# Kernel optimization log

Measured on AMD Instinct MI355X. Metric: run time of the kernel, lower is better.

## Reference

```python
import jax, jax.numpy as jnp
import numpy as np

V = 64                 # |Sigma|
IN_DIM = V + 2         # Sigma + '(' + ')'
OUT_DIM = V + 1        # Sigma + <del>/<end>
H = 512
B = 256
SX = 34                # max proto length 32 + 2 boundaries
SY = 34
BIG_NEG = -1000000000.0


def _one_hot_seq(key, S, batch):
    # '(' at pos 0, L random symbols, ')' at pos L+1, zero padding after
    kl, ks = jax.random.split(key)
    lengths = jax.random.randint(kl, (batch,), 4, S - 1)        # L in [4, S-2]
    syms = jax.random.randint(ks, (S, batch), 0, V)
    pos = jnp.arange(S)[:, None]
    tok = jnp.where(pos == 0, V, jnp.where(pos == lengths[None, :] + 1, V + 1, syms))
    oh = jax.nn.one_hot(tok, IN_DIM, dtype=jnp.float32)
    valid = (pos <= lengths[None, :] + 1).astype(jnp.float32)
    return oh * valid[:, :, None]


def setup_inputs() -> dict:
    key = jax.random.key(0)
    ks = jax.random.split(key, 14)

    def p(k, shape, scale):
        return jax.random.uniform(k, shape, jnp.float32, -scale, scale)

    s = 1.0 / float(np.sqrt(H))
    s2 = 1.0 / float(np.sqrt(2 * H))
    return {
        "sources": _one_hot_seq(ks[0], SX, B),
        "targets": _one_hot_seq(ks[1], SY, B),
        # bidirectional prior LSTM (input IN_DIM -> hidden H, fwd + rev)
        "Wih_f": p(ks[2], (4 * H, IN_DIM), s), "Whh_f": p(ks[3], (4 * H, H), s), "b_f": p(ks[4], (4 * H,), s),
        "Wih_r": p(ks[5], (4 * H, IN_DIM), s), "Whh_r": p(ks[6], (4 * H, H), s), "b_r": p(ks[7], (4 * H,), s),
        # modern LSTM (input IN_DIM -> hidden 2H)
        "Wih_m": p(ks[8], (8 * H, IN_DIM), s2), "Whh_m": p(ks[9], (8 * H, 2 * H), s2), "b_m": p(ks[10], (8 * H,), s2),
        # heads: Linear(2H -> OUT_DIM) + LogSoftmax
        "W_sub": p(ks[11], (OUT_DIM, 2 * H), s2), "b_sub": jnp.zeros((OUT_DIM,), jnp.float32),
        "W_ins": p(ks[12], (OUT_DIM, 2 * H), s2), "b_ins": jnp.zeros((OUT_DIM,), jnp.float32),
    }


def _lstm(x, Wih, Whh, b, hid):
    # torch gate order: i, f, g, o
    bsz = x.shape[1]
    def step(carry, xt):
        h, c = carry
        g = xt @ Wih.T + h @ Whh.T + b
        i, f, gg, o = jnp.split(g, 4, axis=-1)
        c = jax.nn.sigmoid(f) * c + jax.nn.sigmoid(i) * jnp.tanh(gg)
        h = jax.nn.sigmoid(o) * jnp.tanh(c)
        return (h, c), h
    init = (jnp.zeros((bsz, hid), x.dtype), jnp.zeros((bsz, hid), x.dtype))
    _, hs = jax.lax.scan(step, init, x)
    return hs  # [S, B, hid]


def _forward(sources, targets, Wih_f, Whh_f, b_f, Wih_r, Whh_r, b_r,
             Wih_m, Whh_m, b_m, W_sub, b_sub, W_ins, b_ins):
    x_fwd = _lstm(sources, Wih_f, Whh_f, b_f, H)
    x_bwd = _lstm(sources[::-1], Wih_r, Whh_r, b_r, H)[::-1]
    x_emb = jnp.concatenate([x_fwd, x_bwd], axis=-1)   # [SX, B, 2H]
    y_emb = _lstm(targets, Wih_m, Whh_m, b_m, 2 * H)    # [SY, B, 2H]

    # head(x_emb[i] + y_emb[j]) decomposes since Linear is affine
    def pair_logprobs(W, bb):
        lx = jnp.einsum('ibh,oh->ibo', x_emb, W)              # [SX, B, O]
        ly = jnp.einsum('jbh,oh->jbo', y_emb, W) + bb         # [SY, B, O]
        return jax.nn.log_softmax(lx[:, None] + ly[None, :], axis=-1)  # [SX, SY, B, O]

    sub_log = pair_logprobs(W_sub, b_sub)
    ins_log = pair_logprobs(W_ins, b_ins)

    # cell (i, j, b) is computed iff x[i] and y[j] are real (non-padding) one-hots, j <= max_cognat_length
    x_any = sources.sum(-1) > 0                                # [SX, B]
    y_any = targets.sum(-1) > 0                                # [SY, B]
    j_ok = jnp.arange(SY) < SY - 1
    valid = x_any[:, None, :] & (y_any & j_ok[:, None])[None, :, :]   # [SX, SY, B]

    end = jnp.where(valid, ins_log[..., V], BIG_NEG)           # insProbs[V_SIZE]
    dlt = jnp.where(valid, sub_log[..., V], BIG_NEG)           # subProbs[V_SIZE]

    y_next = jnp.pad(targets[1:], ((0, 1), (0, 0), (0, 0)))    # y[j+1], [SY, B, IN_DIM]
    ins_ok = valid & (y_next[..., IN_DIM - 1] == 0)[None]      # not bool(y[j+1, V_SIZE+1])
    ins_val = jnp.einsum('ijbv,jbv->ijb', ins_log[..., :V], y_next[..., :V])
    sub_val = jnp.einsum('ijbv,jbv->ijb', sub_log[..., :V], y_next[..., :V])

    # stacked cached probs: [ins, sub, end, del], each [SX, SY, B]
    return jnp.stack([
        jnp.where(ins_ok, ins_val, BIG_NEG),
        jnp.where(ins_ok, sub_val, BIG_NEG),
        end,
        dlt,
    ])


def reference(sources, targets, Wih_f, Whh_f, b_f, Wih_r, Whh_r, b_r,
              Wih_m, Whh_m, b_m, W_sub, b_sub, W_ins, b_ins):
    return _forward(sources, targets, Wih_f, Whh_f, b_f, Wih_r, Whh_r, b_r,
                    Wih_m, Whh_m, b_m, W_sub, b_sub, W_ins, b_ins)
```

## Files before the change

kernel.cpp:

```cpp
#include <hip/hip_runtime.h>

typedef __attribute__((ext_vector_type(4))) float f32x4;
typedef unsigned char u8;
typedef unsigned long long u64t;

#define BIG_NEG -1000000000.0f

static constexpr int B_  = 256;
static constexpr int SX_ = 34;
static constexpr int SY_ = 34;
static constexpr int IND = 66;
static constexpr int OP_ = 80;

__device__ __forceinline__ f32x4 mfma_fp8(long a, long b, f32x4 c) {
  return __builtin_amdgcn_mfma_f32_16x16x32_fp8_fp8(a, b, c, 0, 0, 0);
}
__device__ __forceinline__ float sigm(float x)  { return 1.0f / (1.0f + __expf(-x)); }
__device__ __forceinline__ float tanhx(float x) { return 2.0f * sigm(2.0f * x) - 1.0f; }
template <bool HI>
__device__ __forceinline__ unsigned pk2(float a, float b, unsigned old) {
  return __builtin_amdgcn_cvt_pk_fp8_f32(a, b, (int)old, HI);
}
__device__ __forceinline__ long pack8(const float* p) {
  float4 f0 = *(const float4*)p;
  float4 f1 = *(const float4*)(p + 4);
  unsigned w0 = pk2<false>(f0.x, f0.y, 0); w0 = pk2<true>(f0.z, f0.w, w0);
  unsigned w1 = pk2<false>(f1.x, f1.y, 0); w1 = pk2<true>(f1.z, f1.w, w1);
  return (long)(((u64t)w1 << 32) | (u64t)w0);
}

__global__ __launch_bounds__(256) void prep_all(
    const float* __restrict__ src, const float* __restrict__ tgt,
    int* __restrict__ tok_x, int* __restrict__ tok_y,
    const float* __restrict__ Wsub, const float* __restrict__ Wins,
    u8* __restrict__ Wcat,
    const float* __restrict__ Wihf, const float* __restrict__ bf,
    const float* __restrict__ Wihr, const float* __restrict__ br,
    const float* __restrict__ Wihm, const float* __restrict__ bm,
    float* __restrict__ Ef, float* __restrict__ Er, float* __restrict__ Em,
    const float* __restrict__ Whm, u8* __restrict__ w8m) {
  __shared__ float tile[64 * 67];
  const int blk = blockIdx.x;
  const int tid = threadIdx.x;

  if (blk < 68) {
    int idx = blk * 256 + tid;
    const int half = SX_ * B_;
    const float* base = (idx < half) ? src : tgt;
    int* outp         = (idx < half) ? tok_x : tok_y;
    int k = (idx < half) ? idx : idx - half;
    const float* p = base + (size_t)k * IND;
    int tok = -1;
    for (int v = 0; v < IND; ++v) if (p[v] > 0.5f) tok = v;
    outp[k] = tok;
  } else if (blk < 228) {
    int widx = (blk - 68) * 256 + tid;
    int row = widx >> 8;
    int wc  = widx & 255;
    int srow = row < 80 ? row : row - 80;
    const float* W = row < 80 ? Wsub : Wins;
    float f0 = 0.f, f1 = 0.f, f2 = 0.f, f3 = 0.f;
    if (srow < 65) {
      const float* p = W + (size_t)srow * 1024 + wc * 4;
      f0 = p[0]; f1 = p[1]; f2 = p[2]; f3 = p[3];
    }
    unsigned w = pk2<false>(f0, f1, 0);
    w = pk2<true>(f2, f3, w);
    ((unsigned*)Wcat)[widx] = w;
  } else if (blk < 356) {
    int tb = blk - 228;
    const float* W; const float* bias; float* E; int H4; int n0;
    if (tb < 32)      { W = Wihf; bias = bf; E = Ef; H4 = 2048; n0 = tb * 64; }
    else if (tb < 64) { W = Wihr; bias = br; E = Er; H4 = 2048; n0 = (tb - 32) * 64; }
    else              { W = Wihm; bias = bm; E = Em; H4 = 4096; n0 = (tb - 64) * 64; }
    const float* s2 = W + (size_t)n0 * IND;
    for (int i = tid; i < 64 * IND; i += 256) {
      int n = i / IND, v = i - n * IND;
      tile[n * 67 + v] = s2[i];
    }
    __syncthreads();
    int lane = tid & 63, w2 = tid >> 6;
    float bl = bias[n0 + lane];
    for (int v = w2; v < 67; v += 4) {
      float val = (v < 66 ? tile[lane * 67 + v] : 0.f) + bl;
      E[(size_t)v * H4 + n0 + lane] = val;
    }
  } else {
    const int M4 = 4096 * 1024 / 4;
    int i = (blk - 356) * 256 + tid;
    int stride = 3072 * 256;
    for (; i < M4; i += stride) {
      float4 f = ((const float4*)Whm)[i];
      unsigned w3 = pk2<false>(f.x, f.y, 0);
      w3 = pk2<true>(f.z, f.w, w3);
      ((unsigned*)w8m)[i] = w3;
    }
  }
}

__device__ __forceinline__ void run_lstm_mod(
    const u8* __restrict__ w8, const float* __restrict__ E,
    u8* __restrict__ hall, int b0, int h0,
    unsigned* __restrict__ dom_flags, int myid,
    u8* __restrict__ alds, u8* __restrict__ hT, const u8* __restrict__ tok_small) {
  constexpr int HH = 1024;
  constexpr int NS = 32;
  const int tid = threadIdx.x;
  const int lane = tid & 63, w = tid >> 6;
  const int lo = lane & 15, q = lane >> 4;
  constexpr int AST2 = HH + 8;
  constexpr int NK = HH / 32;
  const int hh = lo & 7;
  const bool hi = (lo >= 8);
  const int hu_e = h0 + w * 8 + hh;

  long breg0[NK], breg1[NK];
  {
    const u8* brow0 = w8 + (size_t)((lo >> 3) * HH + hu_e) * HH + q * 8;
    const u8* brow1 = w8 + (size_t)((2 + (lo >> 3)) * HH + hu_e) * HH + q * 8;
#pragma unroll
    for (int kk = 0; kk < NK; ++kk) {
      breg0[kk] = *(const long*)(brow0 + kk * 32);
      breg1[kk] = *(const long*)(brow1 + kk * 32);
    }
  }
  float creg[4] = {0.f, 0.f, 0.f, 0.f};

  for (int t = 0; t < 34; ++t) {
    f32x4 acc[2][2];
#pragma unroll
    for (int mt = 0; mt < 2; ++mt) {
      acc[mt][0] = (f32x4){0.f, 0.f, 0.f, 0.f};
      acc[mt][1] = (f32x4){0.f, 0.f, 0.f, 0.f};
    }

    if (t > 0) {
      const u8* hsrc = hall + (size_t)t * (256 * HH);
      u64t tmp[16];
#pragma unroll
      for (int ii = 0; ii < 16; ++ii) {
        int idx = tid + ii * 256;
        tmp[ii] = __hip_atomic_load(
            (const u64t*)(hsrc + (size_t)(b0 + (idx >> 7)) * HH + (idx & 127) * 8),
            __ATOMIC_RELAXED, __HIP_MEMORY_SCOPE_AGENT);
      }
#pragma unroll
      for (int ii = 0; ii < 16; ++ii) {
        int idx = tid + ii * 256;
        *(u64t*)&alds[(idx >> 7) * AST2 + (idx & 127) * 8] = tmp[ii];
      }
      __syncthreads();

      const u8* a0p = alds + lo * AST2 + q * 8;
      const u8* a1p = alds + (16 + lo) * AST2 + q * 8;
#pragma unroll
      for (int kk = 0; kk < NK; ++kk) {
        long a0 = *(const long*)(a0p + kk * 32);
        long a1 = *(const long*)(a1p + kk * 32);
        acc[0][0] = mfma_fp8(a0, breg0[kk], acc[0][0]);
        acc[0][1] = mfma_fp8(a0, breg1[kk], acc[0][1]);
        acc[1][0] = mfma_fp8(a1, breg0[kk], acc[1][0]);
        acc[1][1] = mfma_fp8(a1, breg1[kk], acc[1][1]);
      }
    }

    const u8* tkp = tok_small + t * 32;
#pragma unroll
    for (int mt = 0; mt < 2; ++mt) {
      f32x4 t0 = acc[mt][0], t1 = acc[mt][1];
      f32x4 p0, p1;
#pragma unroll
      for (int c2 = 0; c2 < 4; ++c2) {
        p0[c2] = __shfl_xor(t0[c2], 8, 64);
        p1[c2] = __shfl_xor(t1[c2], 8, 64);
      }
#pragma unroll
      for (int rr = 0; rr < 2; ++rr) {
        int r = (hi ? 2 : 0) + rr;
        float iv = hi ? p0[r] : t0[r];
        float fv = hi ? t0[r] : p0[r];
        float gv = hi ? p1[r] : t1[r];
        float ov = hi ? t1[r] : p1[r];
        int m = mt * 16 + q * 4 + r;
        int v = tkp[m];
        const float* e = E + (size_t)v * (4 * HH) + hu_e;
        iv += e[0]; fv += e[HH]; gv += e[2 * HH]; ov += e[3 * HH];
        float cold = creg[mt * 2 + rr];
        float cn = sigm(fv) * cold + sigm(iv) * tanhx(gv);
        float hn = sigm(ov) * tanhx(cn);
        creg[mt * 2 + rr] = cn;
        hT[m * 32 + w * 8 + hh] = (u8)(pk2<false>(hn, hn, 0) & 0xffu);
      }
    }
    __syncthreads();

    {
      int m = tid >> 3, cc = tid & 7;
      unsigned val = *(const unsigned*)&hT[m * 32 + cc * 4];
      u8* hdst = hall + (size_t)(t + 1) * (256 * HH);
      __hip_atomic_store((unsigned*)(hdst + (size_t)(b0 + m) * HH + h0 + cc * 4),
                         val, __ATOMIC_RELAXED, __HIP_MEMORY_SCOPE_AGENT);
    }

    if (t < 33) {
      __asm__ volatile("s_waitcnt vmcnt(0)" ::: "memory");
      __syncthreads();
      unsigned tgt = (unsigned)(t + 1);
      if (tid == 0)
        __hip_atomic_store(&dom_flags[myid * 32], tgt,
                           __ATOMIC_RELAXED, __HIP_MEMORY_SCOPE_AGENT);
      if (tid < NS) {
        int spin = 0;
        for (;;) {
          unsigned v = __hip_atomic_load(&dom_flags[tid * 32],
                                         __ATOMIC_RELAXED, __HIP_MEMORY_SCOPE_AGENT);
          if (__ballot(v < tgt) == 0) break;
          __builtin_amdgcn_s_sleep(1);
          if (++spin > (1 << 17)) break;
        }
      }
      __syncthreads();
    }
  }
}

__device__ __forceinline__ void run_lstm_fr(
    const float* __restrict__ Whh, const float* __restrict__ E,
    bool revr, u8* __restrict__ hall, int b0, int h0,
    unsigned* __restrict__ dom_flags, int myid,
    u8* __restrict__ alds, u8* __restrict__ hT, const u8* __restrict__ tok_small) {
  constexpr int HH = 512;
  constexpr int NS = 16;
  const int tid = threadIdx.x;
  const int lane = tid & 63, w = tid >> 6;
  const int lo = lane & 15, q = lane >> 4;
  constexpr int AST2 = HH + 8;
  const int hh = lo & 7;
  const bool hi = (lo >= 8);
  const int hu_e = h0 + w * 8 + hh;

  long breg0[16], breg1[16];
  {
    const float* bf0 = Whh + ((size_t)((lo >> 3) * HH + hu_e)) * HH + q * 8;
    const float* bf1 = Whh + ((size_t)((2 + (lo >> 3)) * HH + hu_e)) * HH + q * 8;
#pragma unroll
    for (int kk = 0; kk < 16; ++kk) {
      breg0[kk] = pack8(bf0 + kk * 32);
      breg1[kk] = pack8(bf1 + kk * 32);
    }
  }
  float creg[4] = {0.f, 0.f, 0.f, 0.f};

  for (int t = 0; t < 34; ++t) {
    f32x4 acc[2][2];
#pragma unroll
    for (int mt = 0; mt < 2; ++mt) {
      acc[mt][0] = (f32x4){0.f, 0.f, 0.f, 0.f};
      acc[mt][1] = (f32x4){0.f, 0.f, 0.f, 0.f};
    }

    if (t > 0) {
      const u8* hsrc = hall + (size_t)t * (256 * HH);
      u64t tmp[8];
#pragma unroll
      for (int ii = 0; ii < 8; ++ii) {
        int idx = tid + ii * 256;
        tmp[ii] = __hip_atomic_load(
            (const u64t*)(hsrc + (size_t)(b0 + (idx >> 6)) * HH + (idx & 63) * 8),
            __ATOMIC_RELAXED, __HIP_MEMORY_SCOPE_AGENT);
      }
#pragma unroll
      for (int ii = 0; ii < 8; ++ii) {
        int idx = tid + ii * 256;
        *(u64t*)&alds[(idx >> 6) * AST2 + (idx & 63) * 8] = tmp[ii];
      }
      __syncthreads();

      const u8* a0p = alds + lo * AST2 + q * 8;
      const u8* a1p = alds + (16 + lo) * AST2 + q * 8;
#pragma unroll
      for (int kk = 0; kk < 16; ++kk) {
        long a0 = *(const long*)(a0p + kk * 32);
        long a1 = *(const long*)(a1p + kk * 32);
        acc[0][0] = mfma_fp8(a0, breg0[kk], acc[0][0]);
        acc[0][1] = mfma_fp8(a0, breg1[kk], acc[0][1]);
        acc[1][0] = mfma_fp8(a1, breg0[kk], acc[1][0]);
        acc[1][1] = mfma_fp8(a1, breg1[kk], acc[1][1]);
      }
    }

    int tpos = revr ? 33 - t : t;
    const u8* tkp = tok_small + tpos * 32;
#pragma unroll
    for (int mt = 0; mt < 2; ++mt) {
      f32x4 t0 = acc[mt][0], t1 = acc[mt][1];
      f32x4 p0, p1;
#pragma unroll
      for (int c2 = 0; c2 < 4; ++c2) {
        p0[c2] = __shfl_xor(t0[c2], 8, 64);
        p1[c2] = __shfl_xor(t1[c2], 8, 64);
      }
#pragma unroll
      for (int rr = 0; rr < 2; ++rr) {
        int r = (hi ? 2 : 0) + rr;
        float iv = hi ? p0[r] : t0[r];
        float fv = hi ? t0[r] : p0[r];
        float gv = hi ? p1[r] : t1[r];
        float ov = hi ? t1[r] : p1[r];
        int m = mt * 16 + q * 4 + r;
        int v = tkp[m];
        const float* e = E + (size_t)v * (4 * HH) + hu_e;
        iv += e[0]; fv += e[HH]; gv += e[2 * HH]; ov += e[3 * HH];
        float cold = creg[mt * 2 + rr];
        float cn = sigm(fv) * cold + sigm(iv) * tanhx(gv);
        float hn = sigm(ov) * tanhx(cn);
        creg[mt * 2 + rr] = cn;
        hT[m * 32 + w * 8 + hh] = (u8)(pk2<false>(hn, hn, 0) & 0xffu);
      }
    }
    __syncthreads();

    {
      int m = tid >> 3, cc = tid & 7;
      unsigned val = *(const unsigned*)&hT[m * 32 + cc * 4];
      u8* hdst = hall + (size_t)(t + 1) * (256 * HH);
      __hip_atomic_store((unsigned*)(hdst + (size_t)(b0 + m) * HH + h0 + cc * 4),
                         val, __ATOMIC_RELAXED, __HIP_MEMORY_SCOPE_AGENT);
    }

    if (t < 33) {
      __asm__ volatile("s_waitcnt vmcnt(0)" ::: "memory");
      __syncthreads();
      unsigned tgt = (unsigned)(t + 1);
      if (tid == 0)
        __hip_atomic_store(&dom_flags[myid * 32], tgt,
                           __ATOMIC_RELAXED, __HIP_MEMORY_SCOPE_AGENT);
      if (tid < NS) {
        int spin = 0;
        for (;;) {
          unsigned v = __hip_atomic_load(&dom_flags[tid * 32],
                                         __ATOMIC_RELAXED, __HIP_MEMORY_SCOPE_AGENT);
          if (__ballot(v < tgt) == 0) break;
          __builtin_amdgcn_s_sleep(1);
          if (++spin > (1 << 17)) break;
        }
      }
      __syncthreads();
    }
  }
}

__global__ __launch_bounds__(256, 2) void lstm_persist(
    const int* __restrict__ tok_x, const int* __restrict__ tok_y,
    const float* __restrict__ E_f, const float* __restrict__ Whh_f,
    const float* __restrict__ E_r, const float* __restrict__ Whh_r,
    const float* __restrict__ E_m, const u8* __restrict__ w8_m,
    u8* __restrict__ fwd_all, u8* __restrict__ rev_all, u8* __restrict__ y_all,
    unsigned* __restrict__ flags) {
  __shared__ u8 alds[32 * 1032];
  __shared__ u8 hT[32 * 32];
  __shared__ u8 tok_small[34 * 32];

  const int b = blockIdx.x;
  int role, c, s;
  if (b < 256)      { role = 2; c = b >> 5; s = b & 31; }
  else if (b < 384) { int l = b - 256; role = 0; c = l >> 4; s = l & 15; }
  else              { int l = b - 384; role = 1; c = l >> 4; s = l & 15; }

  u8* hall        = role == 0 ? fwd_all : role == 1 ? rev_all : y_all;
  const int* tokg = (role == 2) ? tok_y : tok_x;
  const int b0 = c * 32;
  const int h0 = s * 32;
  const int dom0 = (role == 2) ? c * 32 : (role == 0) ? 256 + c * 16 : 384 + c * 16;

  for (int i = threadIdx.x; i < 34 * 32; i += 256) {
    int t2 = i >> 5, m = i & 31;
    int tk = tokg[t2 * 256 + b0 + m];
    tok_small[i] = (u8)(tk < 0 ? 66 : tk);
  }
  __syncthreads();

  unsigned* dom_flags = flags + dom0 * 32;
  if (role == 2)
    run_lstm_mod(w8_m, E_m, hall, b0, h0, dom_flags, s, alds, hT, tok_small);
  else if (role == 0)
    run_lstm_fr(Whh_f, E_f, false, hall, b0, h0, dom_flags, s, alds, hT, tok_small);
  else
    run_lstm_fr(Whh_r, E_r, true, hall, b0, h0, dom_flags, s, alds, hT, tok_small);
}

__global__ __launch_bounds__(256, 1) void head_kernel(
    const u8* __restrict__ fwd_all, const u8* __restrict__ rev_all,
    const u8* __restrict__ y_all, const u8* __restrict__ Wcat,
    const float* __restrict__ b_sub, const float* __restrict__ b_ins,
    float* __restrict__ lx_sub, float* __restrict__ lx_ins,
    float* __restrict__ ly_sub, float* __restrict__ ly_ins) {
  __shared__ u8 wq[160 * 264];
  const int lane = threadIdx.x & 63, wave = threadIdx.x >> 6;
  const int lo = lane & 15, q = lane >> 4;
  int blk = blockIdx.x;
  bool yside = (blk >= 136);
  int mb = yside ? blk - 136 : blk;
  int ij = mb >> 2;
  int bbase = (mb & 3) * 64;

  f32x4 acc[10];
#pragma unroll
  for (int nn = 0; nn < 10; ++nn) acc[nn] = (f32x4){0.f,0.f,0.f,0.f};

  for (int qk = 0; qk < 4; ++qk) {
    long aA[8];
    {
      int row = bbase + wave * 16 + lo;
      const u8* ab;
      if (yside)
        ab = y_all + ((size_t)(ij + 1) * 256 + row) * 1024 + qk * 256 + q * 8;
      else if (qk < 2)
        ab = fwd_all + ((size_t)(ij + 1) * 256 + row) * 512 + qk * 256 + q * 8;
      else
        ab = rev_all + ((size_t)(34 - ij) * 256 + row) * 512 + (qk - 2) * 256 + q * 8;
#pragma unroll
      for (int ki = 0; ki < 8; ++ki) aA[ki] = *(const long*)(ab + ki * 32);
    }

    for (int c8 = threadIdx.x; c8 < 160 * 32; c8 += 256) {
      int row = c8 >> 5, col = (c8 & 31) << 3;
      *(long*)&wq[row * 264 + col] =
          *(const long*)&Wcat[(size_t)row * 1024 + qk * 256 + col];
    }
    __syncthreads();

#pragma unroll
    for (int ki = 0; ki < 8; ++ki) {
#pragma unroll
      for (int nn = 0; nn < 10; ++nn) {
        long bf = *(const long*)&wq[(nn * 16 + lo) * 264 + ki * 32 + q * 8];
        acc[nn] = mfma_fp8(aA[ki], bf, acc[nn]);
      }
    }
    __syncthreads();
  }

#pragma unroll
  for (int nn = 0; nn < 10; ++nn) {
    bool is_sub = (nn < 5);
    int n = (is_sub ? nn : nn - 5) * 16 + lo;
    float bias = 0.0f;
    if (yside && n < 65) bias = is_sub ? b_sub[n] : b_ins[n];
    float* dst = yside ? (is_sub ? ly_sub : ly_ins) : (is_sub ? lx_sub : lx_ins);
#pragma unroll
    for (int r = 0; r < 4; ++r) {
      int b = bbase + wave * 16 + q * 4 + r;
      dst[((size_t)ij * 256 + b) * OP_ + n] = acc[nn][r] + bias;
    }
  }
}

__device__ __forceinline__ void lse_one(const float4* __restrict__ X,
                                        const float* __restrict__ py, int sym,
                                        float& logZ, float& v64, float& vs) {
  float v[68];
  const float4* py4 = (const float4*)py;
#pragma unroll
  for (int q = 0; q < 17; ++q) {
    float4 yb = py4[q];
    v[4 * q + 0] = X[q].x + yb.x;
    v[4 * q + 1] = X[q].y + yb.y;
    v[4 * q + 2] = X[q].z + yb.z;
    v[4 * q + 3] = X[q].w + yb.w;
  }
  float m = v[0];
#pragma unroll
  for (int o = 1; o < 65; ++o) m = fmaxf(m, v[o]);
  float s = 0.0f, vsl = 0.0f;
#pragma unroll
  for (int o = 0; o < 65; ++o) {
    s += __expf(v[o] - m);
    if (o < 64) vsl = (o == sym) ? v[o] : vsl;
  }
  logZ = m + __logf(s);
  v64 = v[64];
  vs = vsl;
}

__global__ __launch_bounds__(256, 1) void pair_kernel(
    const int* __restrict__ tok_x, const int* __restrict__ tok_y,
    const float* __restrict__ lx_sub, const float* __restrict__ lx_ins,
    const float* __restrict__ ly_sub, const float* __restrict__ ly_ins,
    float* __restrict__ out) {
  const int hsel = blockIdx.x >= 136;
  const int rem = hsel ? blockIdx.x - 136 : blockIdx.x;
  const int i = rem >> 2;
  const int bc = rem & 3;
  const int jq = threadIdx.x >> 6;
  const int bl = threadIdx.x & 63;
  const int b = bc * 64 + bl;
  const size_t CH = (size_t)SX_ * SY_ * B_;
  const float* lx = hsel ? lx_ins : lx_sub;
  const float* ly = hsel ? ly_ins : ly_sub;
  float* outA = out + (hsel ? 0 : CH);
  float* outB = out + (hsel ? 2 * CH : 3 * CH);

  float4 X[17];
  {
    const float4* ps = (const float4*)(lx + ((size_t)i * 256 + b) * OP_);
#pragma unroll
    for (int q = 0; q < 17; ++q) X[q] = ps[q];
  }
  int tx = tok_x[i * 256 + b];

  for (int j = jq; j < 34; j += 4) {
    size_t obase = ((size_t)i * SY_ + j) * 256 + b;
    bool dead = (j == SY_ - 1) || (tx < 0);
    if (!dead) {
      int ty = tok_y[j * 256 + b];
      if (ty < 0) dead = true;
    }
    if (dead) {
      outA[obase] = BIG_NEG;
      outB[obase] = BIG_NEG;
      continue;
    }
    int tn = tok_y[(j + 1) * 256 + b];
    bool ins_ok = (tn != 65);
    int sym = (tn >= 0 && tn < 64) ? tn : -1;

    float logZ, v64, vs;
    lse_one(X, ly + ((size_t)j * 256 + b) * OP_, sym, logZ, v64, vs);
    float valB = v64 - logZ;
    float valA = (sym >= 0) ? (vs - logZ) : 0.0f;
    outA[obase] = ins_ok ? valA : BIG_NEG;
    outB[obase] = valB;
  }
}

extern "C" void kernel_launch(void* const* d_in, const int* in_sizes, int n_in,
                              void* d_out, int out_size, void* d_ws, size_t ws_size,
                              hipStream_t stream) {
  const float* sources = (const float*)d_in[0];
  const float* targets = (const float*)d_in[1];
  const float* Wih_f = (const float*)d_in[2];
  const float* Whh_f = (const float*)d_in[3];
  const float* b_f   = (const float*)d_in[4];
  const float* Wih_r = (const float*)d_in[5];
  const float* Whh_r = (const float*)d_in[6];
  const float* b_r   = (const float*)d_in[7];
  const float* Wih_m = (const float*)d_in[8];
  const float* Whh_m = (const float*)d_in[9];
  const float* b_m   = (const float*)d_in[10];
  const float* W_sub = (const float*)d_in[11];
  const float* b_sub = (const float*)d_in[12];
  const float* W_ins = (const float*)d_in[13];
  const float* b_ins = (const float*)d_in[14];
  float* out = (float*)d_out;

  char* w = (char*)d_ws;
  constexpr size_t FLAG_SZ = 512 * 32 * 4;
  constexpr size_t TOK_SZ  = (size_t)SX_ * B_ * 4;
  constexpr size_t WCAT_SZ = (size_t)160 * 1024;
  constexpr size_t W8M_SZ  = (size_t)4096 * 1024;
  constexpr size_t EF_SZ   = (size_t)67 * 2048 * 4;
  constexpr size_t EM_SZ   = (size_t)67 * 4096 * 4;
  constexpr size_t LX_SZ   = (size_t)SX_ * B_ * OP_ * 4;
  constexpr size_t HF_SZ   = (size_t)35 * B_ * 512;
  constexpr size_t HM_SZ   = (size_t)35 * B_ * 1024;

  size_t off = 0;
  unsigned* flags = (unsigned*)(w + off); off += FLAG_SZ;
  int*  tok_x   = (int*)(w + off);  off += TOK_SZ;
  int*  tok_y   = (int*)(w + off);  off += TOK_SZ;
  off = (off + 255) & ~(size_t)255;
  u8*   Wcat    = (u8*)(w + off);   off += WCAT_SZ;
  u8*   w8_m    = (u8*)(w + off);   off += W8M_SZ;
  float* E_f    = (float*)(w + off); off += EF_SZ;
  float* E_r    = (float*)(w + off); off += EF_SZ;
  float* E_m    = (float*)(w + off); off += EM_SZ;
  float* lx_sub = (float*)(w + off); off += LX_SZ;
  float* lx_ins = (float*)(w + off); off += LX_SZ;
  float* ly_sub = (float*)(w + off); off += LX_SZ;
  float* ly_ins = (float*)(w + off); off += LX_SZ;
  u8* fwd_all   = (u8*)(w + off);   off += HF_SZ;
  u8* rev_all   = (u8*)(w + off);   off += HF_SZ;
  u8* y_all     = (u8*)(w + off);   off += HM_SZ;
  (void)ws_size; (void)in_sizes; (void)n_in; (void)out_size;

  (void)hipMemsetAsync(flags, 0, FLAG_SZ, stream);

  prep_all<<<3428, 256, 0, stream>>>(
      sources, targets, tok_x, tok_y,
      W_sub, W_ins, Wcat,
      Wih_f, b_f, Wih_r, b_r, Wih_m, b_m, E_f, E_r, E_m,
      Whh_m, w8_m);

  lstm_persist<<<512, 256, 0, stream>>>(
      tok_x, tok_y,
      E_f, Whh_f,
      E_r, Whh_r,
      E_m, w8_m,
      fwd_all, rev_all, y_all, flags);

  head_kernel<<<272, 256, 0, stream>>>(fwd_all, rev_all, y_all, Wcat,
                                       b_sub, b_ins, lx_sub, lx_ins, ly_sub, ly_ins);

  pair_kernel<<<272, 256, 0, stream>>>(tok_x, tok_y, lx_sub, lx_ins,
                                       ly_sub, ly_ins, out);
}
```

Before: 341.0 us.

## Fold input projection into fp8 MFMA via one-hot augmented K, store y-logits as bf16

Instead of gathering fp32 input-projection rows (plus bias) from a precomputed table per timestep, the one-hot token and a constant-1 column are written into an extra 96-byte K segment of the LDS A tile. The matching fp8 Wih and bias columns are appended as three extra MFMA K-steps held in registers. This removes the scattered global gathers in the gate epilogue. The cost is fp8 quantization of Wih and bias, extra register pressure, and a slightly larger LDS tile. Separately, the y-side head logits are stored as bf16 to halve the traffic read by pair_kernel, at some precision loss.

```diff
diff --git a/kernel.cpp b/kernel.cpp
--- a/kernel.cpp
+++ b/kernel.cpp
@@ -2,6 +2,7 @@
 
 typedef __attribute__((ext_vector_type(4))) float f32x4;
 typedef unsigned char u8;
+typedef unsigned short u16;
 typedef unsigned long long u64t;
 
 #define BIG_NEG -1000000000.0f
@@ -11,6 +12,7 @@
 static constexpr int SY_ = 34;
 static constexpr int IND = 66;
 static constexpr int OP_ = 80;
+static constexpr int KE_ = 96;
 
 __device__ __forceinline__ f32x4 mfma_fp8(long a, long b, f32x4 c) {
   return __builtin_amdgcn_mfma_f32_16x16x32_fp8_fp8(a, b, c, 0, 0, 0);
@@ -27,6 +29,13 @@
   unsigned w0 = pk2<false>(f0.x, f0.y, 0); w0 = pk2<true>(f0.z, f0.w, w0);
   unsigned w1 = pk2<false>(f1.x, f1.y, 0); w1 = pk2<true>(f1.z, f1.w, w1);
   return (long)(((u64t)w1 << 32) | (u64t)w0);
+}
+__device__ __forceinline__ u16 f2bf(float f) {
+  unsigned b = __float_as_uint(f) + 0x8000u;
+  return (u16)(b >> 16);
+}
+__device__ __forceinline__ float bf2f(unsigned us) {
+  return __uint_as_float(us << 16);
 }
 
 __global__ __launch_bounds__(256) void prep_all(
@@ -37,9 +46,8 @@
     const float* __restrict__ Wihf, const float* __restrict__ bf,
     const float* __restrict__ Wihr, const float* __restrict__ br,
     const float* __restrict__ Wihm, const float* __restrict__ bm,
-    float* __restrict__ Ef, float* __restrict__ Er, float* __restrict__ Em,
+    u8* __restrict__ w8e,
     const float* __restrict__ Whm, u8* __restrict__ w8m) {
-  __shared__ float tile[64 * 67];
   const int blk = blockIdx.x;
   const int tid = threadIdx.x;
 
@@ -67,28 +75,37 @@
     unsigned w = pk2<false>(f0, f1, 0);
     w = pk2<true>(f2, f3, w);
     ((unsigned*)Wcat)[widx] = w;
-  } else if (blk < 356) {
-    int tb = blk - 228;
-    const float* W; const float* bias; float* E; int H4; int n0;
-    if (tb < 32)      { W = Wihf; bias = bf; E = Ef; H4 = 2048; n0 = tb * 64; }
-    else if (tb < 64) { W = Wihr; bias = br; E = Er; H4 = 2048; n0 = (tb - 32) * 64; }
-    else              { W = Wihm; bias = bm; E = Em; H4 = 4096; n0 = (tb - 64) * 64; }
-    const float* s2 = W + (size_t)n0 * IND;
-    for (int i = tid; i < 64 * IND; i += 256) {
-      int n = i / IND, v = i - n * IND;
-      tile[n * 67 + v] = s2[i];
-    }
-    __syncthreads();
-    int lane = tid & 63, w2 = tid >> 6;
-    float bl = bias[n0 + lane];
-    for (int v = w2; v < 67; v += 4) {
-      float val = (v < 66 ? tile[lane * 67 + v] : 0.f) + bl;
-      E[(size_t)v * H4 + n0 + lane] = val;
+  } else if (blk < 268) {
+    int row = (blk - 228) * 256 + tid;
+    if (row < 8192) {
+      const float* W; const float* bias; int r;
+      if (row < 2048)      { W = Wihf; bias = bf; r = row; }
+      else if (row < 4096) { W = Wihr; bias = br; r = row - 2048; }
+      else                 { W = Wihm; bias = bm; r = row - 4096; }
+      const float* wr = W + (size_t)r * IND;
+      float bv = bias[r];
+      unsigned* dst = (unsigned*)(w8e + (size_t)row * KE_);
+#pragma unroll
+      for (int w4 = 0; w4 < 24; ++w4) {
+        float v0 = 0.f, v1 = 0.f, v2 = 0.f, v3 = 0.f;
+        int c = w4 * 4;
+        if (c + 3 < 66) {
+          v0 = wr[c]; v1 = wr[c + 1]; v2 = wr[c + 2]; v3 = wr[c + 3];
+        } else if (c < 68) {
+          v0 = (c < 66) ? wr[c] : (c == 66 ? bv : 0.f);
+          v1 = (c + 1 < 66) ? wr[c + 1] : (c + 1 == 66 ? bv : 0.f);
+          v2 = (c + 2 < 66) ? wr[c + 2] : (c + 2 == 66 ? bv : 0.f);
+          v3 = (c + 3 < 66) ? wr[c + 3] : (c + 3 == 66 ? bv : 0.f);
+        }
+        unsigned w2 = pk2<false>(v0, v1, 0);
+        w2 = pk2<true>(v2, v3, w2);
+        dst[w4] = w2;
+      }
     }
   } else {
     const int M4 = 4096 * 1024 / 4;
-    int i = (blk - 356) * 256 + tid;
-    int stride = 3072 * 256;
+    int i = (blk - 268) * 256 + tid;
+    int stride = 3160 * 256;
     for (; i < M4; i += stride) {
       float4 f = ((const float4*)Whm)[i];
       unsigned w3 = pk2<false>(f.x, f.y, 0);
@@ -99,22 +116,22 @@
 }
 
 __device__ __forceinline__ void run_lstm_mod(
-    const u8* __restrict__ w8, const float* __restrict__ E,
+    const u8* __restrict__ w8, const u8* __restrict__ w8e,
     u8* __restrict__ hall, int b0, int h0,
     unsigned* __restrict__ dom_flags, int myid,
     u8* __restrict__ alds, u8* __restrict__ hT, const u8* __restrict__ tok_small) {
   constexpr int HH = 1024;
   constexpr int NS = 32;
+  constexpr int NK = 32;
   const int tid = threadIdx.x;
   const int lane = tid & 63, w = tid >> 6;
   const int lo = lane & 15, q = lane >> 4;
-  constexpr int AST2 = HH + 8;
-  constexpr int NK = HH / 32;
+  constexpr int AST2 = HH + KE_ + 8;
   const int hh = lo & 7;
   const bool hi = (lo >= 8);
   const int hu_e = h0 + w * 8 + hh;
 
-  long breg0[NK], breg1[NK];
+  long breg0[NK + 3], breg1[NK + 3];
   {
     const u8* brow0 = w8 + (size_t)((lo >> 3) * HH + hu_e) * HH + q * 8;
     const u8* brow1 = w8 + (size_t)((2 + (lo >> 3)) * HH + hu_e) * HH + q * 8;
@@ -123,17 +140,25 @@
       breg0[kk] = *(const long*)(brow0 + kk * 32);
       breg1[kk] = *(const long*)(brow1 + kk * 32);
     }
+    const u8* e0 = w8e + (size_t)((lo >> 3) * HH + hu_e) * KE_ + q * 8;
+    const u8* e1 = w8e + (size_t)((2 + (lo >> 3)) * HH + hu_e) * KE_ + q * 8;
+#pragma unroll
+    for (int e = 0; e < 3; ++e) {
+      breg0[NK + e] = *(const long*)(e0 + e * 32);
+      breg1[NK + e] = *(const long*)(e1 + e * 32);
+    }
   }
   float creg[4] = {0.f, 0.f, 0.f, 0.f};
 
   for (int t = 0; t < 34; ++t) {
-    f32x4 acc[2][2];
-#pragma unroll
-    for (int mt = 0; mt < 2; ++mt) {
-      acc[mt][0] = (f32x4){0.f, 0.f, 0.f, 0.f};
-      acc[mt][1] = (f32x4){0.f, 0.f, 0.f, 0.f};
-    }
-
+    if (tid < 32) {
+      u8* rowp = alds + tid * AST2 + HH;
+#pragma unroll
+      for (int w8i = 0; w8i < 12; ++w8i) *(u64t*)(rowp + 8 * w8i) = 0;
+      int v = tok_small[t * 32 + tid];
+      if (v < 66) rowp[v] = 0x38;
+      rowp[66] = 0x38;
+    }
     if (t > 0) {
       const u8* hsrc = hall + (size_t)t * (256 * HH);
       u64t tmp[16];
@@ -149,10 +174,18 @@
         int idx = tid + ii * 256;
         *(u64t*)&alds[(idx >> 7) * AST2 + (idx & 127) * 8] = tmp[ii];
       }
-      __syncthreads();
-
-      const u8* a0p = alds + lo * AST2 + q * 8;
-      const u8* a1p = alds + (16 + lo) * AST2 + q * 8;
+    }
+    __syncthreads();
+
+    f32x4 acc[2][2];
+#pragma unroll
+    for (int mt = 0; mt < 2; ++mt) {
+      acc[mt][0] = (f32x4){0.f, 0.f, 0.f, 0.f};
+      acc[mt][1] = (f32x4){0.f, 0.f, 0.f, 0.f};
+    }
+    const u8* a0p = alds + lo * AST2 + q * 8;
+    const u8* a1p = alds + (16 + lo) * AST2 + q * 8;
+    if (t > 0) {
 #pragma unroll
       for (int kk = 0; kk < NK; ++kk) {
         long a0 = *(const long*)(a0p + kk * 32);
@@ -163,8 +196,16 @@
         acc[1][1] = mfma_fp8(a1, breg1[kk], acc[1][1]);
       }
     }
-
-    const u8* tkp = tok_small + t * 32;
+#pragma unroll
+    for (int kk = NK; kk < NK + 3; ++kk) {
+      long a0 = *(const long*)(a0p + kk * 32);
+      long a1 = *(const long*)(a1p + kk * 32);
+      acc[0][0] = mfma_fp8(a0, breg0[kk], acc[0][0]);
+      acc[0][1] = mfma_fp8(a0, breg1[kk], acc[0][1]);
+      acc[1][0] = mfma_fp8(a1, breg0[kk], acc[1][0]);
+      acc[1][1] = mfma_fp8(a1, breg1[kk], acc[1][1]);
+    }
+
 #pragma unroll
     for (int mt = 0; mt < 2; ++mt) {
       f32x4 t0 = acc[mt][0], t1 = acc[mt][1];
@@ -182,9 +223,6 @@
         float gv = hi ? p1[r] : t1[r];
         float ov = hi ? t1[r] : p1[r];
         int m = mt * 16 + q * 4 + r;
-        int v = tkp[m];
-        const float* e = E + (size_t)v * (4 * HH) + hu_e;
-        iv += e[0]; fv += e[HH]; gv += e[2 * HH]; ov += e[3 * HH];
         float cold = creg[mt * 2 + rr];
         float cn = sigm(fv) * cold + sigm(iv) * tanhx(gv);
         float hn = sigm(ov) * tanhx(cn);
@@ -225,40 +263,50 @@
 }
 
 __device__ __forceinline__ void run_lstm_fr(
-    const float* __restrict__ Whh, const float* __restrict__ E,
+    const float* __restrict__ Whh, const u8* __restrict__ w8e,
     bool revr, u8* __restrict__ hall, int b0, int h0,
     unsigned* __restrict__ dom_flags, int myid,
     u8* __restrict__ alds, u8* __restrict__ hT, const u8* __restrict__ tok_small) {
   constexpr int HH = 512;
   constexpr int NS = 16;
+  constexpr int NK = 16;
   const int tid = threadIdx.x;
   const int lane = tid & 63, w = tid >> 6;
   const int lo = lane & 15, q = lane >> 4;
-  constexpr int AST2 = HH + 8;
+  constexpr int AST2 = HH + KE_ + 8;
   const int hh = lo & 7;
   const bool hi = (lo >= 8);
   const int hu_e = h0 + w * 8 + hh;
 
-  long breg0[16], breg1[16];
+  long breg0[NK + 3], breg1[NK + 3];
   {
     const float* bf0 = Whh + ((size_t)((lo >> 3) * HH + hu_e)) * HH + q * 8;
     const float* bf1 = Whh + ((size_t)((2 + (lo >> 3)) * HH + hu_e)) * HH + q * 8;
 #pragma unroll
-    for (int kk = 0; kk < 16; ++kk) {
+    for (int kk = 0; kk < NK; ++kk) {
       breg0[kk] = pack8(bf0 + kk * 32);
       breg1[kk] = pack8(bf1 + kk * 32);
     }
+    const u8* e0 = w8e + (size_t)((lo >> 3) * HH + hu_e) * KE_ + q * 8;
+    const u8* e1 = w8e + (size_t)((2 + (lo >> 3)) * HH + hu_e) * KE_ + q * 8;
+#pragma unroll
+    for (int e = 0; e < 3; ++e) {
+      breg0[NK + e] = *(const long*)(e0 + e * 32);
+      breg1[NK + e] = *(const long*)(e1 + e * 32);
+    }
   }
   float creg[4] = {0.f, 0.f, 0.f, 0.f};
 
   for (int t = 0; t < 34; ++t) {
-    f32x4 acc[2][2];
-#pragma unroll
-    for (int mt = 0; mt < 2; ++mt) {
-      acc[mt][0] = (f32x4){0.f, 0.f, 0.f, 0.f};
-      acc[mt][1] = (f32x4){0.f, 0.f, 0.f, 0.f};
-    }
-
+    int tpos = revr ? 33 - t : t;
+    if (tid < 32) {
+      u8* rowp = alds + tid * AST2 + HH;
+#pragma unroll
+      for (int w8i = 0; w8i < 12; ++w8i) *(u64t*)(rowp + 8 * w8i) = 0;
+      int v = tok_small[tpos * 32 + tid];
+      if (v < 66) rowp[v] = 0x38;
+      rowp[66] = 0x38;
+    }
     if (t > 0) {
       const u8* hsrc = hall + (size_t)t * (256 * HH);
       u64t tmp[8];
@@ -274,12 +322,20 @@
         int idx = tid + ii * 256;
         *(u64t*)&alds[(idx >> 6) * AST2 + (idx & 63) * 8] = tmp[ii];
       }
-      __syncthreads();
-
-      const u8* a0p = alds + lo * AST2 + q * 8;
-      const u8* a1p = alds + (16 + lo) * AST2 + q * 8;
-#pragma unroll
-      for (int kk = 0; kk < 16; ++kk) {
+    }
+    __syncthreads();
+
+    f32x4 acc[2][2];
+#pragma unroll
+    for (int mt = 0; mt < 2; ++mt) {
+      acc[mt][0] = (f32x4){0.f, 0.f, 0.f, 0.f};
+      acc[mt][1] = (f32x4){0.f, 0.f, 0.f, 0.f};
+    }
+    const u8* a0p = alds + lo * AST2 + q * 8;
+    const u8* a1p = alds + (16 + lo) * AST2 + q * 8;
+    if (t > 0) {
+#pragma unroll
+      for (int kk = 0; kk < NK; ++kk) {
         long a0 = *(const long*)(a0p + kk * 32);
         long a1 = *(const long*)(a1p + kk * 32);
         acc[0][0] = mfma_fp8(a0, breg0[kk], acc[0][0]);
@@ -288,9 +344,16 @@
         acc[1][1] = mfma_fp8(a1, breg1[kk], acc[1][1]);
       }
     }
-
-    int tpos = revr ? 33 - t : t;
-    const u8* tkp = tok_small + tpos * 32;
+#pragma unroll
+    for (int kk = NK; kk < NK + 3; ++kk) {
+      long a0 = *(const long*)(a0p + kk * 32);
+      long a1 = *(const long*)(a1p + kk * 32);
+      acc[0][0] = mfma_fp8(a0, breg0[kk], acc[0][0]);
+      acc[0][1] = mfma_fp8(a0, breg1[kk], acc[0][1]);
+      acc[1][0] = mfma_fp8(a1, breg0[kk], acc[1][0]);
+      acc[1][1] = mfma_fp8(a1, breg1[kk], acc[1][1]);
+    }
+
 #pragma unroll
     for (int mt = 0; mt < 2; ++mt) {
       f32x4 t0 = acc[mt][0], t1 = acc[mt][1];
@@ -308,9 +371,6 @@
         float gv = hi ? p1[r] : t1[r];
         float ov = hi ? t1[r] : p1[r];
         int m = mt * 16 + q * 4 + r;
-        int v = tkp[m];
-        const float* e = E + (size_t)v * (4 * HH) + hu_e;
-        iv += e[0]; fv += e[HH]; gv += e[2 * HH]; ov += e[3 * HH];
         float cold = creg[mt * 2 + rr];
         float cn = sigm(fv) * cold + sigm(iv) * tanhx(gv);
         float hn = sigm(ov) * tanhx(cn);
@@ -352,12 +412,11 @@
 
 __global__ __launch_bounds__(256, 2) void lstm_persist(
     const int* __restrict__ tok_x, const int* __restrict__ tok_y,
-    const float* __restrict__ E_f, const float* __restrict__ Whh_f,
-    const float* __restrict__ E_r, const float* __restrict__ Whh_r,
-    const float* __restrict__ E_m, const u8* __restrict__ w8_m,
+    const float* __restrict__ Whh_f, const float* __restrict__ Whh_r,
+    const u8* __restrict__ w8_m, const u8* __restrict__ w8e,
     u8* __restrict__ fwd_all, u8* __restrict__ rev_all, u8* __restrict__ y_all,
     unsigned* __restrict__ flags) {
-  __shared__ u8 alds[32 * 1032];
+  __shared__ u8 alds[32 * 1128];
   __shared__ u8 hT[32 * 32];
   __shared__ u8 tok_small[34 * 32];
 
@@ -382,11 +441,13 @@
 
   unsigned* dom_flags = flags + dom0 * 32;
   if (role == 2)
-    run_lstm_mod(w8_m, E_m, hall, b0, h0, dom_flags, s, alds, hT, tok_small);
+    run_lstm_mod(w8_m, w8e + (size_t)4096 * KE_ * 1, hall, b0, h0, dom_flags, s,
+                 alds, hT, tok_small);
   else if (role == 0)
-    run_lstm_fr(Whh_f, E_f, false, hall, b0, h0, dom_flags, s, alds, hT, tok_small);
+    run_lstm_fr(Whh_f, w8e, false, hall, b0, h0, dom_flags, s, alds, hT, tok_small);
   else
-    run_lstm_fr(Whh_r, E_r, true, hall, b0, h0, dom_flags, s, alds, hT, tok_small);
+    run_lstm_fr(Whh_r, w8e + (size_t)2048 * KE_, true, hall, b0, h0, dom_flags, s,
+                alds, hT, tok_small);
 }
 
 __global__ __launch_bounds__(256, 1) void head_kernel(
@@ -394,7 +455,7 @@
     const u8* __restrict__ y_all, const u8* __restrict__ Wcat,
     const float* __restrict__ b_sub, const float* __restrict__ b_ins,
     float* __restrict__ lx_sub, float* __restrict__ lx_ins,
-    float* __restrict__ ly_sub, float* __restrict__ ly_ins) {
+    u16* __restrict__ ly_sub, u16* __restrict__ ly_ins) {
   __shared__ u8 wq[160 * 264];
   const int lane = threadIdx.x & 63, wave = threadIdx.x >> 6;
   const int lo = lane & 15, q = lane >> 4;
@@ -445,48 +506,29 @@
   for (int nn = 0; nn < 10; ++nn) {
     bool is_sub = (nn < 5);
     int n = (is_sub ? nn : nn - 5) * 16 + lo;
-    float bias = 0.0f;
-    if (yside && n < 65) bias = is_sub ? b_sub[n] : b_ins[n];
-    float* dst = yside ? (is_sub ? ly_sub : ly_ins) : (is_sub ? lx_sub : lx_ins);
-#pragma unroll
-    for (int r = 0; r < 4; ++r) {
-      int b = bbase + wave * 16 + q * 4 + r;
-      dst[((size_t)ij * 256 + b) * OP_ + n] = acc[nn][r] + bias;
-    }
-  }
-}
-
-__device__ __forceinline__ void lse_one(const float4* __restrict__ X,
-                                        const float* __restrict__ py, int sym,
-                                        float& logZ, float& v64, float& vs) {
-  float v[68];
-  const float4* py4 = (const float4*)py;
-#pragma unroll
-  for (int q = 0; q < 17; ++q) {
-    float4 yb = py4[q];
-    v[4 * q + 0] = X[q].x + yb.x;
-    v[4 * q + 1] = X[q].y + yb.y;
-    v[4 * q + 2] = X[q].z + yb.z;
-    v[4 * q + 3] = X[q].w + yb.w;
-  }
-  float m = v[0];
-#pragma unroll
-  for (int o = 1; o < 65; ++o) m = fmaxf(m, v[o]);
-  float s = 0.0f, vsl = 0.0f;
-#pragma unroll
-  for (int o = 0; o < 65; ++o) {
-    s += __expf(v[o] - m);
-    if (o < 64) vsl = (o == sym) ? v[o] : vsl;
-  }
-  logZ = m + __logf(s);
-  v64 = v[64];
-  vs = vsl;
+    if (yside) {
+      float bias = (n < 65) ? (is_sub ? b_sub[n] : b_ins[n]) : 0.0f;
+      u16* dst = is_sub ? ly_sub : ly_ins;
+#pragma unroll
+      for (int r = 0; r < 4; ++r) {
+        int b = bbase + wave * 16 + q * 4 + r;
+        dst[((size_t)ij * 256 + b) * OP_ + n] = f2bf(acc[nn][r] + bias);
+      }
+    } else {
+      float* dst = is_sub ? lx_sub : lx_ins;
+#pragma unroll
+      for (int r = 0; r < 4; ++r) {
+        int b = bbase + wave * 16 + q * 4 + r;
+        dst[((size_t)ij * 256 + b) * OP_ + n] = acc[nn][r];
+      }
+    }
+  }
 }
 
 __global__ __launch_bounds__(256, 1) void pair_kernel(
     const int* __restrict__ tok_x, const int* __restrict__ tok_y,
     const float* __restrict__ lx_sub, const float* __restrict__ lx_ins,
-    const float* __restrict__ ly_sub, const float* __restrict__ ly_ins,
+    const u16* __restrict__ ly_sub, const u16* __restrict__ ly_ins,
     float* __restrict__ out) {
   const int hsel = blockIdx.x >= 136;
   const int rem = hsel ? blockIdx.x - 136 : blockIdx.x;
@@ -497,7 +539,7 @@
   const int b = bc * 64 + bl;
   const size_t CH = (size_t)SX_ * SY_ * B_;
   const float* lx = hsel ? lx_ins : lx_sub;
-  const float* ly = hsel ? ly_ins : ly_sub;
+  const u16* ly = hsel ? ly_ins : ly_sub;
   float* outA = out + (hsel ? 0 : CH);
   float* outB = out + (hsel ? 2 * CH : 3 * CH);
 
@@ -525,10 +567,30 @@
     bool ins_ok = (tn != 65);
     int sym = (tn >= 0 && tn < 64) ? tn : -1;
 
-    float logZ, v64, vs;
-    lse_one(X, ly + ((size_t)j * 256 + b) * OP_, sym, logZ, v64, vs);
-    float valB = v64 - logZ;
-    float valA = (sym >= 0) ? (vs - logZ) : 0.0f;
+    float v[68];
+    {
+      const u64t* py = (const u64t*)(ly + ((size_t)j * 256 + b) * OP_);
+#pragma unroll
+      for (int q2 = 0; q2 < 17; ++q2) {
+        u64t y = py[q2];
+        v[4 * q2 + 0] = X[q2].x + bf2f((unsigned)(y & 0xffffu));
+        v[4 * q2 + 1] = X[q2].y + bf2f((unsigned)((y >> 16) & 0xffffu));
+        v[4 * q2 + 2] = X[q2].z + bf2f((unsigned)((y >> 32) & 0xffffu));
+        v[4 * q2 + 3] = X[q2].w + bf2f((unsigned)(y >> 48));
+      }
+    }
+    float m = v[0];
+#pragma unroll
+    for (int o = 1; o < 65; ++o) m = fmaxf(m, v[o]);
+    float s = 0.0f, vsl = 0.0f;
+#pragma unroll
+    for (int o = 0; o < 65; ++o) {
+      s += __expf(v[o] - m);
+      if (o < 64) vsl = (o == sym) ? v[o] : vsl;
+    }
+    float logZ = m + __logf(s);
+    float valB = v[64] - logZ;
+    float valA = (sym >= 0) ? (vsl - logZ) : 0.0f;
     outA[obase] = ins_ok ? valA : BIG_NEG;
     outB[obase] = valB;
   }
@@ -559,9 +621,9 @@
   constexpr size_t TOK_SZ  = (size_t)SX_ * B_ * 4;
   constexpr size_t WCAT_SZ = (size_t)160 * 1024;
   constexpr size_t W8M_SZ  = (size_t)4096 * 1024;
-  constexpr size_t EF_SZ   = (size_t)67 * 2048 * 4;
-  constexpr size_t EM_SZ   = (size_t)67 * 4096 * 4;
+  constexpr size_t W8E_SZ  = (size_t)8192 * KE_;
   constexpr size_t LX_SZ   = (size_t)SX_ * B_ * OP_ * 4;
+  constexpr size_t LY_SZ   = (size_t)SX_ * B_ * OP_ * 2;
   constexpr size_t HF_SZ   = (size_t)35 * B_ * 512;
   constexpr size_t HM_SZ   = (size_t)35 * B_ * 1024;
 
@@ -572,13 +634,12 @@
   off = (off + 255) & ~(size_t)255;
   u8*   Wcat    = (u8*)(w + off);   off += WCAT_SZ;
   u8*   w8_m    = (u8*)(w + off);   off += W8M_SZ;
-  float* E_f    = (float*)(w + off); off += EF_SZ;
-  float* E_r    = (float*)(w + off); off += EF_SZ;
-  float* E_m    = (float*)(w + off); off += EM_SZ;
+  u8*   w8e     = (u8*)(w + off);   off += W8E_SZ;
   float* lx_sub = (float*)(w + off); off += LX_SZ;
   float* lx_ins = (float*)(w + off); off += LX_SZ;
-  float* ly_sub = (float*)(w + off); off += LX_SZ;
-  float* ly_ins = (float*)(w + off); off += LX_SZ;
+  u16*  ly_sub  = (u16*)(w + off);  off += LY_SZ;
+  u16*  ly_ins  = (u16*)(w + off);  off += LY_SZ;
+  off = (off + 255) & ~(size_t)255;
   u8* fwd_all   = (u8*)(w + off);   off += HF_SZ;
   u8* rev_all   = (u8*)(w + off);   off += HF_SZ;
   u8* y_all     = (u8*)(w + off);   off += HM_SZ;
@@ -589,14 +650,13 @@
   prep_all<<<3428, 256, 0, stream>>>(
       sources, targets, tok_x, tok_y,
       W_sub, W_ins, Wcat,
-      Wih_f, b_f, Wih_r, b_r, Wih_m, b_m, E_f, E_r, E_m,
+      Wih_f, b_f, Wih_r, b_r, Wih_m, b_m, w8e,
       Whh_m, w8_m);
 
   lstm_persist<<<512, 256, 0, stream>>>(
       tok_x, tok_y,
-      E_f, Whh_f,
-      E_r, Whh_r,
-      E_m, w8_m,
+      Whh_f, Whh_r,
+      w8_m, w8e,
       fwd_all, rev_all, y_all, flags);
 
   head_kernel<<<272, 256, 0, stream>>>(fwd_all, rev_all, y_all, Wcat,
```

New measurement: 347.3 us. No clear change (+1.8%).
